# Kernel tuning notes

Measured on AMD Instinct MI355X. Metric: run time of the kernel, lower is better.

## Reference

```python
import jax, jax.numpy as jnp
import numpy as np

LN_EPS = 1e-5


def setup_inputs() -> dict:
    key = jax.random.key(0)
    ks = jax.random.split(key, 10)
    B, C, H, W = 4, 128, 64, 64
    N = H * W
    return {
        "prompt_feat": jax.random.normal(ks[0], (B, C, H, W), jnp.float32),
        "x": jax.random.normal(ks[1], (B, C, H, W), jnp.float32),
        "Wq": jax.random.normal(ks[2], (C, C), jnp.float32) * (1.0 / np.sqrt(C)),
        "bq": jax.random.normal(ks[3], (C,), jnp.float32) * 0.01,
        "Wk": jax.random.normal(ks[4], (C, C), jnp.float32) * (1.0 / np.sqrt(C)),
        "bk": jax.random.normal(ks[5], (C,), jnp.float32) * 0.01,
        "Wv": jax.random.normal(ks[6], (C, C), jnp.float32) * (1.0 / np.sqrt(C)),
        "bv": jax.random.normal(ks[7], (C,), jnp.float32) * 0.01,
        "gamma": jnp.ones((C,), jnp.float32),
        "beta": jnp.zeros((C,), jnp.float32),
        "mask_bits": jax.random.randint(ks[8], (B, N), 0, 2, jnp.int32),
    }


def reference(prompt_feat, x, Wq, bq, Wk, bk, Wv, bv, gamma, beta, mask_bits):
    B, C, H, W = x.shape
    N = H * W
    # (B, C, H, W) -> (B, N, C) token layout
    xs = x.reshape(B, C, N).transpose(0, 2, 1)
    ps = prompt_feat.reshape(B, C, N).transpose(0, 2, 1)
    # QKV projections (torch Linear: y = x @ W.T + b)
    Q = ps @ Wq.T + bq
    K = xs @ Wk.T + bk
    V = xs @ Wv.T + bv
    # full NxN scores with additive key mask (0 where bit set, -inf otherwise)
    scores = jnp.einsum("bnc,bmc->bnm", Q, K) / jnp.sqrt(jnp.asarray(C, scores_dtype := Q.dtype))
    add_mask = jnp.where(mask_bits > 0, jnp.asarray(0.0, scores_dtype), jnp.asarray(-jnp.inf, scores_dtype))
    scores = scores + add_mask[:, None, :]
    attn = jax.nn.softmax(scores, axis=-1)
    out = jnp.einsum("bnm,bmc->bnc", attn, V) + xs  # residual
    # LayerNorm over channels
    mu = jnp.mean(out, axis=-1, keepdims=True)
    var = jnp.mean(jnp.square(out - mu), axis=-1, keepdims=True)
    out = (out - mu) * jax.lax.rsqrt(var + LN_EPS) * gamma + beta
    return out.transpose(0, 2, 1).reshape(B, C, H, W)
```

## Files before the change

### kernel.cpp

```cpp
#include <hip/hip_runtime.h>


#define CCH 128
#define NTOK 4096
#define FM 16.0f

typedef __attribute__((ext_vector_type(8))) short  bf16x8;
typedef __attribute__((ext_vector_type(4))) short  bf16x4;
typedef __attribute__((ext_vector_type(4))) float  f32x4;

__device__ __forceinline__ f32x4 mfma16(bf16x4 a, bf16x4 b, f32x4 c) {
    return __builtin_amdgcn_mfma_f32_16x16x16bf16_1k(a, b, c, 0, 0, 0);
}

__device__ __forceinline__ unsigned short f2bf(float f) {
    unsigned int u = __builtin_bit_cast(unsigned int, f);
    u += 0x7FFFu + ((u >> 16) & 1u);
    return (unsigned short)(u >> 16);
}
__device__ __forceinline__ unsigned int pack2bf(float a, float b) {
    return (unsigned int)f2bf(a) | ((unsigned int)f2bf(b) << 16);
}
__device__ __forceinline__ void gload_lds16(const void* g, void* l) {
    __builtin_amdgcn_global_load_lds(
        (const __attribute__((address_space(1))) unsigned int*)g,
        (__attribute__((address_space(3))) unsigned int*)l, 16, 0, 0);
}

__device__ __forceinline__ void stageW(char* Wb, const float* __restrict__ W, int t) {
    const int co = t >> 1, h = t & 1;
    const float4* src = reinterpret_cast<const float4*>(W + co * CCH + h * 64);
    char* row = Wb + co * 256;
    const int sw = (co & 7) << 3;
    #pragma unroll
    for (int q = 0; q < 16; ++q) {
        const float4 v = src[q];
        const int c2 = h * 32 + q * 2;
        *reinterpret_cast<unsigned int*>(row + (((c2    ) ^ sw) << 2)) = pack2bf(v.x, v.y);
        *reinterpret_cast<unsigned int*>(row + (((c2 + 1) ^ sw) << 2)) = pack2bf(v.z, v.w);
    }
}

__global__ __launch_bounds__(256) void qkv_kernel(
    const float* __restrict__ prompt, const float* __restrict__ xg,
    const float* __restrict__ Wq, const float* __restrict__ bq,
    const float* __restrict__ Wk, const float* __restrict__ bk,
    const float* __restrict__ Wv, const float* __restrict__ bv,
    unsigned short* __restrict__ Qo, unsigned short* __restrict__ Ko,
    unsigned short* __restrict__ Vo)
{
    extern __shared__ __align__(16) char qpool[];
    char* pT = qpool;
    char* xT = qpool + 16384;
    char* Wb = qpool + 32768;

    const int t  = threadIdx.x;
    const int b  = blockIdx.x >> 6;
    const int n0 = (blockIdx.x & 63) << 6;
    const int l  = t & 63;
    const int w  = t >> 6;
    const int g  = l >> 4;
    const int lr = l & 15;

    {
        const int c2 = t & 63, th = t >> 6;
        const float* ps = prompt + (((size_t)b * CCH + 2 * c2) << 12) + n0 + th * 16;
        const float* xs = xg     + (((size_t)b * CCH + 2 * c2) << 12) + n0 + th * 16;
        float pa[16], pb[16], xa[16], xb[16];
        #pragma unroll
        for (int q = 0; q < 4; ++q) {
            *reinterpret_cast<float4*>(&pa[q*4]) = *reinterpret_cast<const float4*>(ps + q*4);
            *reinterpret_cast<float4*>(&pb[q*4]) = *reinterpret_cast<const float4*>(ps + 4096 + q*4);
            *reinterpret_cast<float4*>(&xa[q*4]) = *reinterpret_cast<const float4*>(xs + q*4);
            *reinterpret_cast<float4*>(&xb[q*4]) = *reinterpret_cast<const float4*>(xs + 4096 + q*4);
        }
        #pragma unroll
        for (int j = 0; j < 16; ++j) {
            const int tok = th * 16 + j;
            const int off = tok * 256 + (((c2) ^ ((tok & 7) << 3)) << 2);
            *reinterpret_cast<unsigned int*>(pT + off) = pack2bf(pa[j], pb[j]);
            *reinterpret_cast<unsigned int*>(xT + off) = pack2bf(xa[j], xb[j]);
        }
    }
    stageW(Wb, Wq, t);
    __syncthreads();

    const float SC2 = 0.12754849f;
    const int swl = (lr & 7) << 3;

    {
        bf16x8 af[4];
        #pragma unroll
        for (int s = 0; s < 4; ++s)
            af[s] = *reinterpret_cast<const bf16x8*>(
                pT + (w * 16 + lr) * 256 + (((s * 16 + g * 4) ^ swl) << 2));
        f32x4 acc[8];
        #pragma unroll
        for (int cf = 0; cf < 8; ++cf) acc[cf] = (f32x4){0.f,0.f,0.f,0.f};
        #pragma unroll
        for (int cf = 0; cf < 8; ++cf)
            #pragma unroll
            for (int s = 0; s < 4; ++s) {
                bf16x8 bf = *reinterpret_cast<const bf16x8*>(
                    Wb + (cf * 16 + lr) * 256 + (((s * 16 + g * 4) ^ swl) << 2));
                acc[cf] = __builtin_amdgcn_mfma_f32_16x16x32_bf16(af[s], bf, acc[cf], 0, 0, 0);
            }
        #pragma unroll
        for (int cf = 0; cf < 8; ++cf) {
            const float bb = bq[cf * 16 + lr];
            #pragma unroll
            for (int i = 0; i < 4; ++i) {
                const int tok = w * 16 + g * 4 + i;
                Qo[((size_t)(b * NTOK + n0 + tok) << 7) + cf * 16 + lr] =
                    f2bf((acc[cf][i] + bb) * SC2);
            }
        }
    }
    __syncthreads();
    stageW(Wb, Wk, t);
    __syncthreads();

    bf16x8 af[4];
    #pragma unroll
    for (int s = 0; s < 4; ++s)
        af[s] = *reinterpret_cast<const bf16x8*>(
            xT + (w * 16 + lr) * 256 + (((s * 16 + g * 4) ^ swl) << 2));
    {
        f32x4 acc[8];
        #pragma unroll
        for (int cf = 0; cf < 8; ++cf) acc[cf] = (f32x4){0.f,0.f,0.f,0.f};
        #pragma unroll
        for (int cf = 0; cf < 8; ++cf)
            #pragma unroll
            for (int s = 0; s < 4; ++s) {
                bf16x8 bf = *reinterpret_cast<const bf16x8*>(
                    Wb + (cf * 16 + lr) * 256 + (((s * 16 + g * 4) ^ swl) << 2));
                acc[cf] = __builtin_amdgcn_mfma_f32_16x16x32_bf16(af[s], bf, acc[cf], 0, 0, 0);
            }
        #pragma unroll
        for (int cf = 0; cf < 8; ++cf) {
            const float bb = bk[cf * 16 + lr];
            #pragma unroll
            for (int i = 0; i < 4; ++i) {
                const int tok = w * 16 + g * 4 + i;
                Ko[((size_t)(b * NTOK + n0 + tok) << 7) + cf * 16 + lr] =
                    f2bf(acc[cf][i] + bb);
            }
        }
    }
    __syncthreads();
    stageW(Wb, Wv, t);
    __syncthreads();

    {
        f32x4 acc[8];
        #pragma unroll
        for (int cf = 0; cf < 8; ++cf) acc[cf] = (f32x4){0.f,0.f,0.f,0.f};
        #pragma unroll
        for (int cf = 0; cf < 8; ++cf)
            #pragma unroll
            for (int s = 0; s < 4; ++s) {
                bf16x8 bf = *reinterpret_cast<const bf16x8*>(
                    Wb + (cf * 16 + lr) * 256 + (((s * 16 + g * 4) ^ swl) << 2));
                acc[cf] = __builtin_amdgcn_mfma_f32_16x16x32_bf16(af[s], bf, acc[cf], 0, 0, 0);
            }
        #pragma unroll
        for (int cf = 0; cf < 8; ++cf) {
            const float bb = bv[cf * 16 + lr];
            unsigned short pk[4];
            #pragma unroll
            for (int i = 0; i < 4; ++i) pk[i] = f2bf(acc[cf][i] + bb);
            *reinterpret_cast<unsigned long long*>(
                Vo + (((size_t)(b * CCH + cf * 16 + lr)) << 12) + n0 + w * 16 + g * 4) =
                *reinterpret_cast<unsigned long long*>(pk);
        }
    }
}

__device__ __forceinline__ void stage_tile(
    const unsigned short* __restrict__ Kg, const unsigned short* __restrict__ Vg,
    char* KsB, char* VsB, int b, int m0, int w4, int l)
{
    #pragma unroll
    for (int ii = 0; ii < 4; ++ii) {
        const int i = w4 * 4 + ii;
        const int r = i * 4 + (l >> 4);
        const int csrc = (l & 15) ^ (r & 7);
        const unsigned short* src = Kg + ((size_t)(b * NTOK + m0 + r) << 7) + csrc * 8;
        gload_lds16(src, KsB + i * 1024);
    }
    #pragma unroll
    for (int ii = 0; ii < 4; ++ii) {
        const int i = w4 * 4 + ii;
        const int r = i * 8 + (l >> 3);
        const int csrc = (l & 7) ^ (r & 7);
        const unsigned short* src = Vg + ((size_t)(b * CCH + r) << 12) + m0 + csrc * 8;
        gload_lds16(src, VsB + i * 1024);
    }
}

__global__ __launch_bounds__(512) void attn_ln_kernel(
    const unsigned short* __restrict__ Qg, const unsigned short* __restrict__ Kg,
    const unsigned short* __restrict__ Vg,
    const int* __restrict__ maskb, const float* __restrict__ xg,
    const float* __restrict__ gamma, const float* __restrict__ beta,
    float* __restrict__ out)
{
    extern __shared__ __align__(16) char pool[];

    const int bid = (blockIdx.x & 7) * 32 + (blockIdx.x >> 3);
    const int t  = threadIdx.x;
    const int b  = bid >> 6;
    const int n0 = (bid & 63) << 6;
    const int l  = t & 63;
    const int wq = t >> 6;
    const int h  = wq >> 2;
    const int kj2 = (wq >> 1) & 1;
    const int qh = wq & 1;
    const int w4 = wq & 3;
    const int g  = l >> 4;
    const int lr = l & 15;
    const int swz = (lr & 7) << 4;
    const int base_m = h << 11;

    char* KsH = pool + h * 65536;
    char* VsH = pool + h * 65536 + 32768;

    bf16x8 qf[2][4];
    #pragma unroll
    for (int rf = 0; rf < 2; ++rf) {
        const unsigned short* qp =
            Qg + ((size_t)(b * NTOK + n0 + qh * 32 + rf * 16 + lr)) * CCH + g * 8;
        #pragma unroll
        for (int s = 0; s < 4; ++s)
            qf[rf][s] = *reinterpret_cast<const bf16x8*>(qp + s * 32);
    }

    f32x4 acc[2][8];
    float lrun[2] = {0.f, 0.f};
    #pragma unroll
    for (int rf = 0; rf < 2; ++rf)
        #pragma unroll
        for (int cf = 0; cf < 8; ++cf) acc[rf][cf] = (f32x4){0.f,0.f,0.f,0.f};

    stage_tile(Kg, Vg, KsH, VsH, b, base_m, w4, l);

    for (int it = 0; it < 32; ++it) {
        __builtin_amdgcn_s_barrier();
        __builtin_amdgcn_sched_barrier(0);

        const int m0 = base_m + (it << 6);
        const int4 mv0 = *reinterpret_cast<const int4*>(
            maskb + (size_t)b * NTOK + m0 + kj2 * 32 + g * 4);
        const int4 mv1 = *reinterpret_cast<const int4*>(
            maskb + (size_t)b * NTOK + m0 + kj2 * 32 + 16 + g * 4);

        const int tn = (it + 1) & 31;
        stage_tile(Kg, Vg, KsH + (tn & 1) * 16384, VsH + (tn & 1) * 16384,
                   b, base_m + (tn << 6), w4, l);

        asm volatile("s_waitcnt vmcnt(10)" ::: "memory");
        __builtin_amdgcn_sched_barrier(0);
        __builtin_amdgcn_s_barrier();
        __builtin_amdgcn_sched_barrier(0);

        const char* Ks_c = KsH + (it & 1) * 16384;
        const char* Vs_c = VsH + (it & 1) * 16384;

        f32x4 sf[2][2];
        #pragma unroll
        for (int rf = 0; rf < 2; ++rf)
            #pragma unroll
            for (int sub = 0; sub < 2; ++sub)
                sf[rf][sub] = (f32x4){-FM, -FM, -FM, -FM};
        #pragma unroll
        for (int sub = 0; sub < 2; ++sub) {
            const char* rp = Ks_c + (kj2 * 32 + sub * 16 + lr) * 256;
            #pragma unroll
            for (int s = 0; s < 4; ++s) {
                bf16x8 kb = *reinterpret_cast<const bf16x8*>(rp + ((s * 64 + g * 16) ^ swz));
                sf[0][sub] = __builtin_amdgcn_mfma_f32_16x16x32_bf16(kb, qf[0][s], sf[0][sub], 0, 0, 0);
                sf[1][sub] = __builtin_amdgcn_mfma_f32_16x16x32_bf16(kb, qf[1][s], sf[1][sub], 0, 0, 0);
            }
        }

        bf16x4 pb[2][2];
        #pragma unroll
        for (int rf = 0; rf < 2; ++rf) {
            #pragma unroll
            for (int sub = 0; sub < 2; ++sub) {
                const int4 mv = sub ? mv1 : mv0;
                const float p0 = mv.x ? exp2f(sf[rf][sub][0]) : 0.f;
                const float p1 = mv.y ? exp2f(sf[rf][sub][1]) : 0.f;
                const float p2 = mv.z ? exp2f(sf[rf][sub][2]) : 0.f;
                const float p3 = mv.w ? exp2f(sf[rf][sub][3]) : 0.f;
                lrun[rf] += (p0 + p1) + (p2 + p3);
                const unsigned w0 = __builtin_amdgcn_perm(
                    __builtin_bit_cast(unsigned, p1), __builtin_bit_cast(unsigned, p0),
                    0x07060302u);
                const unsigned w1 = __builtin_amdgcn_perm(
                    __builtin_bit_cast(unsigned, p3), __builtin_bit_cast(unsigned, p2),
                    0x07060302u);
                const unsigned long long pk =
                    (unsigned long long)w0 | ((unsigned long long)w1 << 32);
                pb[rf][sub] = __builtin_bit_cast(bf16x4, pk);
            }
        }

        #pragma unroll
        for (int sub = 0; sub < 2; ++sub) {
            const int s16 = kj2 * 2 + sub;
            #pragma unroll
            for (int cf = 0; cf < 8; ++cf) {
                const bf16x4 vb = *reinterpret_cast<const bf16x4*>(
                    Vs_c + (cf * 16 + lr) * 128 +
                    ((((s16 * 2 + (g >> 1)) ^ (lr & 7)) << 4) + ((g & 1) << 3)));
                acc[0][cf] = mfma16(vb, pb[0][sub], acc[0][cf]);
                acc[1][cf] = mfma16(vb, pb[1][sub], acc[1][cf]);
            }
        }
    }

    asm volatile("s_waitcnt vmcnt(0)" ::: "memory");
    #pragma unroll
    for (int rf = 0; rf < 2; ++rf) {
        lrun[rf] += __shfl_xor(lrun[rf], 16);
        lrun[rf] += __shfl_xor(lrun[rf], 32);
    }
    __syncthreads();

    const int sub4 = wq >> 1;
    float* mrg = (float*)pool;
    float* stg = (float*)(pool + 105984);

    if (sub4 != 0) {
        float* dst = mrg + ((sub4 - 1) * 2 + qh) * 4416 + l * 69;
        #pragma unroll
        for (int rf = 0; rf < 2; ++rf)
            #pragma unroll
            for (int cf = 0; cf < 8; ++cf)
                #pragma unroll
                for (int i = 0; i < 4; ++i)
                    dst[rf * 32 + cf * 4 + i] = acc[rf][cf][i];
        dst[64] = lrun[0]; dst[65] = lrun[1];
    }
    {
        const int c = t >> 2, h0 = (t & 3) << 4;
        const float* src = xg + (((size_t)b * CCH + c) << 12) + n0 + h0;
        float* dst = stg + c * 65 + h0;
        #pragma unroll
        for (int k = 0; k < 16; k += 4) {
            const float4 v = *reinterpret_cast<const float4*>(src + k);
            dst[k] = v.x; dst[k+1] = v.y; dst[k+2] = v.z; dst[k+3] = v.w;
        }
    }
    __syncthreads();

    if (sub4 == 0) {
        const float* r1 = mrg + (0 * 2 + qh) * 4416 + l * 69;
        const float* r2 = mrg + (1 * 2 + qh) * 4416 + l * 69;
        const float* r3 = mrg + (2 * 2 + qh) * 4416 + l * 69;
        float gm[8][4], bt[8][4];
        #pragma unroll
        for (int cf = 0; cf < 8; ++cf)
            #pragma unroll
            for (int i = 0; i < 4; ++i) {
                gm[cf][i] = gamma[cf * 16 + g * 4 + i];
                bt[cf][i] = beta [cf * 16 + g * 4 + i];
            }
        #pragma unroll
        for (int rf = 0; rf < 2; ++rf) {
            const float inv = 1.f / (lrun[rf] + r1[64 + rf] + r2[64 + rf] + r3[64 + rf]);
            const int nloc = qh * 32 + rf * 16 + lr;
            float sum = 0.f, sq = 0.f;
            #pragma unroll
            for (int cf = 0; cf < 8; ++cf)
                #pragma unroll
                for (int i = 0; i < 4; ++i) {
                    const int idx = rf * 32 + cf * 4 + i;
                    const float o = acc[rf][cf][i] + r1[idx] + r2[idx] + r3[idx];
                    const float v = o * inv + stg[(cf * 16 + g * 4 + i) * 65 + nloc];
                    acc[rf][cf][i] = v; sum += v; sq += v * v;
                }
            sum += __shfl_xor(sum, 16); sq += __shfl_xor(sq, 16);
            sum += __shfl_xor(sum, 32); sq += __shfl_xor(sq, 32);
            const float mean = sum * (1.f / 128.f);
            const float var  = sq * (1.f / 128.f) - mean * mean;
            const float rstd = rsqrtf(var + 1e-5f);
            #pragma unroll
            for (int cf = 0; cf < 8; ++cf)
                #pragma unroll
                for (int i = 0; i < 4; ++i)
                    stg[(cf * 16 + g * 4 + i) * 65 + nloc] =
                        (acc[rf][cf][i] - mean) * rstd * gm[cf][i] + bt[cf][i];
        }
    }
    __syncthreads();

    {
        const int c = t >> 2, h0 = (t & 3) << 4;
        float* dst = out + (((size_t)b * CCH + c) << 12) + n0 + h0;
        const float* srcl = stg + c * 65 + h0;
        #pragma unroll
        for (int k = 0; k < 16; k += 4) {
            float4 v; v.x = srcl[k]; v.y = srcl[k+1]; v.z = srcl[k+2]; v.w = srcl[k+3];
            *reinterpret_cast<float4*>(dst + k) = v;
        }
    }
}

extern "C" void kernel_launch(void* const* d_in, const int* in_sizes, int n_in,
                              void* d_out, int out_size, void* d_ws, size_t ws_size,
                              hipStream_t stream) {
    const float* prompt = (const float*)d_in[0];
    const float* x      = (const float*)d_in[1];
    const float* Wq     = (const float*)d_in[2];
    const float* bq     = (const float*)d_in[3];
    const float* Wk     = (const float*)d_in[4];
    const float* bk     = (const float*)d_in[5];
    const float* Wv     = (const float*)d_in[6];
    const float* bv     = (const float*)d_in[7];
    const float* gamma  = (const float*)d_in[8];
    const float* beta   = (const float*)d_in[9];
    const int*   maskb  = (const int*)d_in[10];
    float* out = (float*)d_out;

    const size_t M = (size_t)4 * NTOK * CCH;
    unsigned short* Qw = (unsigned short*)d_ws;
    unsigned short* Kw = Qw + M;
    unsigned short* Vw = Kw + M;

    (void)hipFuncSetAttribute((const void*)qkv_kernel,
                              hipFuncAttributeMaxDynamicSharedMemorySize, 65536);
    (void)hipFuncSetAttribute((const void*)attn_ln_kernel,
                              hipFuncAttributeMaxDynamicSharedMemorySize, 139264);

    qkv_kernel<<<256, 256, 65536, stream>>>(prompt, x, Wq, bq, Wk, bk, Wv, bv, Qw, Kw, Vw);
    attn_ln_kernel<<<256, 512, 139264, stream>>>(Qw, Kw, Vw, maskb, x, gamma, beta, out);
}
```

Baseline: 94.46 us.

## Load V fragments directly from global into registers, drop V LDS staging

V tiles are no longer staged through LDS with global_load_lds. Each wave now loads its bf16x4 V fragments straight from global memory into double-buffered registers (vbA/vbB), and the loop is unrolled by two to ping-pong between them. The aim is to cut the LDS footprint and LDS read traffic for V and shorten the per-tile sync path. In exchange it raises register pressure with 32 extra bf16x4 values and many more small, less coalesced global loads whose latency must be hidden by vmcnt(44).

```diff
diff --git a/kernel.cpp b/kernel.cpp
--- a/kernel.cpp
+++ b/kernel.cpp
@@ -177,9 +177,8 @@
     }
 }
 
-__device__ __forceinline__ void stage_tile(
-    const unsigned short* __restrict__ Kg, const unsigned short* __restrict__ Vg,
-    char* KsB, char* VsB, int b, int m0, int w4, int l)
+__device__ __forceinline__ void stageK(
+    const unsigned short* __restrict__ Kg, char* KsB, int b, int m0, int w4, int l)
 {
     #pragma unroll
     for (int ii = 0; ii < 4; ++ii) {
@@ -189,14 +188,72 @@
         const unsigned short* src = Kg + ((size_t)(b * NTOK + m0 + r) << 7) + csrc * 8;
         gload_lds16(src, KsB + i * 1024);
     }
-    #pragma unroll
-    for (int ii = 0; ii < 4; ++ii) {
-        const int i = w4 * 4 + ii;
-        const int r = i * 8 + (l >> 3);
-        const int csrc = (l & 7) ^ (r & 7);
-        const unsigned short* src = Vg + ((size_t)(b * CCH + r) << 12) + m0 + csrc * 8;
-        gload_lds16(src, VsB + i * 1024);
-    }
+}
+
+__device__ __forceinline__ void loadV(
+    const unsigned short* __restrict__ Vbase, bf16x4 (&vb)[2][8],
+    int m0, int kj2, int g, int lr)
+{
+    #pragma unroll
+    for (int sub = 0; sub < 2; ++sub)
+        #pragma unroll
+        for (int cf = 0; cf < 8; ++cf)
+            vb[sub][cf] = *reinterpret_cast<const bf16x4*>(
+                Vbase + (((size_t)(cf * 16 + lr)) << 12) + m0 + kj2 * 32 + sub * 16 + g * 4);
+}
+
+__device__ __forceinline__ void compute_tile(
+    const char* Ks_c, const bf16x4 (&vb)[2][8], int4 mv0, int4 mv1,
+    const bf16x8 (&qf)[2][4], f32x4 (&acc)[2][8], float (&lrun)[2],
+    int kj2, int g, int lr, int swz)
+{
+    f32x4 sf[2][2];
+    #pragma unroll
+    for (int rf = 0; rf < 2; ++rf)
+        #pragma unroll
+        for (int sub = 0; sub < 2; ++sub)
+            sf[rf][sub] = (f32x4){-FM, -FM, -FM, -FM};
+    #pragma unroll
+    for (int sub = 0; sub < 2; ++sub) {
+        const char* rp = Ks_c + (kj2 * 32 + sub * 16 + lr) * 256;
+        #pragma unroll
+        for (int s = 0; s < 4; ++s) {
+            bf16x8 kb = *reinterpret_cast<const bf16x8*>(rp + ((s * 64 + g * 16) ^ swz));
+            sf[0][sub] = __builtin_amdgcn_mfma_f32_16x16x32_bf16(kb, qf[0][s], sf[0][sub], 0, 0, 0);
+            sf[1][sub] = __builtin_amdgcn_mfma_f32_16x16x32_bf16(kb, qf[1][s], sf[1][sub], 0, 0, 0);
+        }
+    }
+
+    bf16x4 pb[2][2];
+    #pragma unroll
+    for (int rf = 0; rf < 2; ++rf) {
+        #pragma unroll
+        for (int sub = 0; sub < 2; ++sub) {
+            const int4 mv = sub ? mv1 : mv0;
+            const float p0 = mv.x ? exp2f(sf[rf][sub][0]) : 0.f;
+            const float p1 = mv.y ? exp2f(sf[rf][sub][1]) : 0.f;
+            const float p2 = mv.z ? exp2f(sf[rf][sub][2]) : 0.f;
+            const float p3 = mv.w ? exp2f(sf[rf][sub][3]) : 0.f;
+            lrun[rf] += (p0 + p1) + (p2 + p3);
+            const unsigned w0 = __builtin_amdgcn_perm(
+                __builtin_bit_cast(unsigned, p1), __builtin_bit_cast(unsigned, p0),
+                0x07060302u);
+            const unsigned w1 = __builtin_amdgcn_perm(
+                __builtin_bit_cast(unsigned, p3), __builtin_bit_cast(unsigned, p2),
+                0x07060302u);
+            const unsigned long long pk =
+                (unsigned long long)w0 | ((unsigned long long)w1 << 32);
+            pb[rf][sub] = __builtin_bit_cast(bf16x4, pk);
+        }
+    }
+
+    #pragma unroll
+    for (int sub = 0; sub < 2; ++sub)
+        #pragma unroll
+        for (int cf = 0; cf < 8; ++cf) {
+            acc[0][cf] = mfma16(vb[sub][cf], pb[0][sub], acc[0][cf]);
+            acc[1][cf] = mfma16(vb[sub][cf], pb[1][sub], acc[1][cf]);
+        }
 }
 
 __global__ __launch_bounds__(512) void attn_ln_kernel(
@@ -223,8 +280,7 @@
     const int swz = (lr & 7) << 4;
     const int base_m = h << 11;
 
-    char* KsH = pool + h * 65536;
-    char* VsH = pool + h * 65536 + 32768;
+    char* KsH = pool + h * 32768;
 
     bf16x8 qf[2][4];
     #pragma unroll
@@ -243,82 +299,54 @@
         #pragma unroll
         for (int cf = 0; cf < 8; ++cf) acc[rf][cf] = (f32x4){0.f,0.f,0.f,0.f};
 
-    stage_tile(Kg, Vg, KsH, VsH, b, base_m, w4, l);
-
-    for (int it = 0; it < 32; ++it) {
+    const int* mb = maskb + (size_t)b * NTOK + base_m + kj2 * 32 + g * 4;
+    const unsigned short* Vbase = Vg + ((size_t)(b * CCH) << 12);
+
+    bf16x4 vbA[2][8], vbB[2][8];
+    int4 mA0, mA1, mB0, mB1;
+
+    stageK(Kg, KsH, b, base_m, w4, l);
+    __builtin_amdgcn_sched_barrier(0);
+    loadV(Vbase, vbA, base_m, kj2, g, lr);
+    mA0 = *reinterpret_cast<const int4*>(mb);
+    mA1 = *reinterpret_cast<const int4*>(mb + 16);
+    __builtin_amdgcn_sched_barrier(0);
+
+    for (int it = 0; it < 32; it += 2) {
         __builtin_amdgcn_s_barrier();
         __builtin_amdgcn_sched_barrier(0);
-
-        const int m0 = base_m + (it << 6);
-        const int4 mv0 = *reinterpret_cast<const int4*>(
-            maskb + (size_t)b * NTOK + m0 + kj2 * 32 + g * 4);
-        const int4 mv1 = *reinterpret_cast<const int4*>(
-            maskb + (size_t)b * NTOK + m0 + kj2 * 32 + 16 + g * 4);
-
-        const int tn = (it + 1) & 31;
-        stage_tile(Kg, Vg, KsH + (tn & 1) * 16384, VsH + (tn & 1) * 16384,
-                   b, base_m + (tn << 6), w4, l);
-
-        asm volatile("s_waitcnt vmcnt(10)" ::: "memory");
+        {
+            const int tm = base_m + ((it + 1) << 6);
+            stageK(Kg, KsH + 16384, b, tm, w4, l);
+            __builtin_amdgcn_sched_barrier(0);
+            loadV(Vbase, vbB, tm, kj2, g, lr);
+            mB0 = *reinterpret_cast<const int4*>(mb + ((it + 1) << 6));
+            mB1 = *reinterpret_cast<const int4*>(mb + ((it + 1) << 6) + 16);
+            __builtin_amdgcn_sched_barrier(0);
+        }
+        asm volatile("s_waitcnt vmcnt(44)" ::: "memory");
         __builtin_amdgcn_sched_barrier(0);
         __builtin_amdgcn_s_barrier();
         __builtin_amdgcn_sched_barrier(0);
-
-        const char* Ks_c = KsH + (it & 1) * 16384;
-        const char* Vs_c = VsH + (it & 1) * 16384;
-
-        f32x4 sf[2][2];
-        #pragma unroll
-        for (int rf = 0; rf < 2; ++rf)
-            #pragma unroll
-            for (int sub = 0; sub < 2; ++sub)
-                sf[rf][sub] = (f32x4){-FM, -FM, -FM, -FM};
-        #pragma unroll
-        for (int sub = 0; sub < 2; ++sub) {
-            const char* rp = Ks_c + (kj2 * 32 + sub * 16 + lr) * 256;
-            #pragma unroll
-            for (int s = 0; s < 4; ++s) {
-                bf16x8 kb = *reinterpret_cast<const bf16x8*>(rp + ((s * 64 + g * 16) ^ swz));
-                sf[0][sub] = __builtin_amdgcn_mfma_f32_16x16x32_bf16(kb, qf[0][s], sf[0][sub], 0, 0, 0);
-                sf[1][sub] = __builtin_amdgcn_mfma_f32_16x16x32_bf16(kb, qf[1][s], sf[1][sub], 0, 0, 0);
-            }
-        }
-
-        bf16x4 pb[2][2];
-        #pragma unroll
-        for (int rf = 0; rf < 2; ++rf) {
-            #pragma unroll
-            for (int sub = 0; sub < 2; ++sub) {
-                const int4 mv = sub ? mv1 : mv0;
-                const float p0 = mv.x ? exp2f(sf[rf][sub][0]) : 0.f;
-                const float p1 = mv.y ? exp2f(sf[rf][sub][1]) : 0.f;
-                const float p2 = mv.z ? exp2f(sf[rf][sub][2]) : 0.f;
-                const float p3 = mv.w ? exp2f(sf[rf][sub][3]) : 0.f;
-                lrun[rf] += (p0 + p1) + (p2 + p3);
-                const unsigned w0 = __builtin_amdgcn_perm(
-                    __builtin_bit_cast(unsigned, p1), __builtin_bit_cast(unsigned, p0),
-                    0x07060302u);
-                const unsigned w1 = __builtin_amdgcn_perm(
-                    __builtin_bit_cast(unsigned, p3), __builtin_bit_cast(unsigned, p2),
-                    0x07060302u);
-                const unsigned long long pk =
-                    (unsigned long long)w0 | ((unsigned long long)w1 << 32);
-                pb[rf][sub] = __builtin_bit_cast(bf16x4, pk);
-            }
-        }
-
-        #pragma unroll
-        for (int sub = 0; sub < 2; ++sub) {
-            const int s16 = kj2 * 2 + sub;
-            #pragma unroll
-            for (int cf = 0; cf < 8; ++cf) {
-                const bf16x4 vb = *reinterpret_cast<const bf16x4*>(
-                    Vs_c + (cf * 16 + lr) * 128 +
-                    ((((s16 * 2 + (g >> 1)) ^ (lr & 7)) << 4) + ((g & 1) << 3)));
-                acc[0][cf] = mfma16(vb, pb[0][sub], acc[0][cf]);
-                acc[1][cf] = mfma16(vb, pb[1][sub], acc[1][cf]);
-            }
-        }
+        compute_tile(KsH, vbA, mA0, mA1, qf, acc, lrun, kj2, g, lr, swz);
+
+        __builtin_amdgcn_s_barrier();
+        __builtin_amdgcn_sched_barrier(0);
+        {
+            const int tn2 = (it + 2) & 31;
+            const int tm = base_m + (tn2 << 6);
+            stageK(Kg, KsH, b, tm, w4, l);
+            __builtin_amdgcn_sched_barrier(0);
+            loadV(Vbase, vbA, tm, kj2, g, lr);
+            mA0 = *reinterpret_cast<const int4*>(mb + (tn2 << 6));
+            mA1 = *reinterpret_cast<const int4*>(mb + (tn2 << 6) + 16);
+            __builtin_amdgcn_sched_barrier(0);
+        }
+        asm volatile("s_waitcnt vmcnt(44)" ::: "memory");
+        __builtin_amdgcn_sched_barrier(0);
+        __builtin_amdgcn_s_barrier();
+        __builtin_amdgcn_sched_barrier(0);
+        compute_tile(KsH + 16384, vbB, mB0, mB1, qf, acc, lrun, kj2, g, lr, swz);
     }
 
     asm volatile("s_waitcnt vmcnt(0)" ::: "memory");
```

New measurement: 215.7 us. 128% more time.
